# Kernel tuning notes

Hardware: AMD Instinct MI355X
Metric: run time of the kernel (lower is better)

Reference implementation:

```python
import jax, jax.numpy as jnp
import numpy as np

DIM = 768
HEADS = 12
DIM_HEAD = 64
INNER = HEADS * DIM_HEAD  # 768
SCALE = DIM_HEAD ** -0.5


def setup_inputs() -> dict:
    key = jax.random.key(0)
    k1, k2, k3, k4 = jax.random.split(key, 4)
    b, n = 8, 1024
    x = jax.random.normal(k1, (b, n, DIM), dtype=jnp.float32)
    # fused QKV projection, no bias: y = x @ w_qkv  -> [b, n, 3*inner]
    w_qkv = jax.random.normal(k2, (DIM, 3 * INNER), dtype=jnp.float32) * (DIM ** -0.5)
    # output projection with bias
    w_out = jax.random.normal(k3, (INNER, DIM), dtype=jnp.float32) * (INNER ** -0.5)
    b_out = jax.random.normal(k4, (DIM,), dtype=jnp.float32) * 0.02
    return {"x": x, "w_qkv": w_qkv, "w_out": w_out, "b_out": b_out}


def reference(x, w_qkv, w_out, b_out):
    b, n, _ = x.shape
    qkv = jnp.einsum('bnd,de->bne', x, w_qkv)  # [b, n, 3*inner]
    q, k, v = jnp.split(qkv, 3, axis=-1)
    # 'b n (h d) -> b h n d'
    def split_heads(t):
        return t.reshape(b, n, HEADS, DIM_HEAD).transpose(0, 2, 1, 3)
    q, k, v = split_heads(q), split_heads(k), split_heads(v)
    dots = jnp.einsum('bhid,bhjd->bhij', q, k) * SCALE  # [b, h, n, n]
    attn = jax.nn.softmax(dots, axis=-1)
    out = jnp.einsum('bhij,bhjd->bhid', attn, v)  # [b, h, n, d]
    out = out.transpose(0, 2, 1, 3).reshape(b, n, INNER)  # 'b h n d -> b n (h d)'
    return jnp.einsum('bne,ed->bnd', out, w_out) + b_out
```

## Files before the change

### kernel.cpp

```cpp
#include <hip/hip_runtime.h>

typedef unsigned short u16;
typedef __bf16 bf16x8 __attribute__((ext_vector_type(8)));
typedef float f32x4 __attribute__((ext_vector_type(4)));

__device__ inline u16 f2bf(float f) {
    union { float f; unsigned int u; } a; a.f = f;
    unsigned int u = a.u + 0x7fffu + ((a.u >> 16) & 1u);
    return (u16)(u >> 16);
}
__device__ __forceinline__ float truncbf(float f, u16& h) {
    union { float f; unsigned int u; } a; a.f = f;
    a.u &= 0xffff0000u;
    h = (u16)(a.u >> 16);
    return a.f;
}

__device__ __forceinline__ void cp16(const void* g, void* l) {
    __builtin_amdgcn_global_load_lds(
        (const __attribute__((address_space(1))) unsigned int*)g,
        (__attribute__((address_space(3))) unsigned int*)l, 16, 0, 0);
}

__global__ __launch_bounds__(256) void prep(
    const float* __restrict__ x, const float* __restrict__ wq,
    const float* __restrict__ wo, u16* __restrict__ xbf,
    u16* __restrict__ wtq, u16* __restrict__ wto)
{
    int bid = blockIdx.x;
    if (bid < 3072) {
        size_t base = ((size_t)bid * 256 + threadIdx.x) * 8;
        float4 f0 = *(const float4*)&x[base];
        float4 f1 = *(const float4*)&x[base + 4];
        union { u16 s[8]; uint4 v; } t;
        t.s[0]=f2bf(f0.x); t.s[1]=f2bf(f0.y); t.s[2]=f2bf(f0.z); t.s[3]=f2bf(f0.w);
        t.s[4]=f2bf(f1.x); t.s[5]=f2bf(f1.y); t.s[6]=f2bf(f1.z); t.s[7]=f2bf(f1.w);
        *(uint4*)&xbf[base] = t.v;
        return;
    }
    __shared__ u16 tile[32][33];
    const float* in; u16* outp; int N, bx, by;
    if (bid < 3072 + 1728) { int t = bid - 3072; in = wq; outp = wtq; N = 2304; bx = t % 72; by = t / 72; }
    else                   { int t = bid - 4800; in = wo; outp = wto; N = 768;  bx = t % 24; by = t / 24; }
    int n0 = bx * 32, k0 = by * 32;
    int tx = threadIdx.x & 31, ty = threadIdx.x >> 5;
    #pragma unroll
    for (int r = ty; r < 32; r += 8)
        tile[r][tx] = f2bf(in[(size_t)(k0 + r) * N + n0 + tx]);
    __syncthreads();
    #pragma unroll
    for (int r = ty; r < 32; r += 8)
        outp[(size_t)(n0 + r) * 768 + k0 + tx] = tile[tx][r];
}

__global__ __launch_bounds__(256) void gemm_qkv(
    const u16* __restrict__ A, const u16* __restrict__ Bt,
    u16* __restrict__ q_out, u16* __restrict__ k_out, u16* __restrict__ v_out)
{
    const int K = 768;
    __shared__ __align__(16) u16 As[2][128 * 64];
    __shared__ __align__(16) u16 Bs[2][128 * 64];

    int tid = threadIdx.x;
    int lane = tid & 63, wave = tid >> 6;
    int quad = lane >> 4, l16 = lane & 15;
    int wm = wave >> 1, wn = wave & 1;
    int id = blockIdx.x;
    int xcd = id & 7, j = id >> 3;
    int m0 = (((j & 7) << 3) + xcd) * 128;
    int n0 = (j >> 3) * 128;

    f32x4 acc[4][4];
    #pragma unroll
    for (int i = 0; i < 4; i++)
        #pragma unroll
        for (int jj = 0; jj < 4; jj++) acc[i][jj] = (f32x4){0.f, 0.f, 0.f, 0.f};

    int r0 = tid >> 3, cg = tid & 7;
    int g = cg ^ (r0 & 7);
    const u16* GA[4]; const u16* GB[4];
    #pragma unroll
    for (int it = 0; it < 4; it++) {
        GA[it] = A  + (size_t)(m0 + it * 32 + r0) * K + g * 8;
        GB[it] = Bt + (size_t)(n0 + it * 32 + r0) * K + g * 8;
    }

    #define STAGE_QKV(kt, b)                                          \
        _Pragma("unroll")                                             \
        for (int it = 0; it < 4; it++) {                              \
            cp16(GA[it] + (kt), &As[b][(it * 256 + tid) * 8]);        \
            cp16(GB[it] + (kt), &Bs[b][(it * 256 + tid) * 8]);        \
        }

    STAGE_QKV(0, 0)
    for (int i = 0; i < 12; i++) {
        int b = i & 1;
        if (i + 1 < 12) {
            STAGE_QKV((i + 1) * 64, b ^ 1)
            asm volatile("s_waitcnt vmcnt(8)" ::: "memory");
        } else {
            asm volatile("s_waitcnt vmcnt(0)" ::: "memory");
        }
        __builtin_amdgcn_s_barrier();
        bf16x8 af[2][4], bfr[2][4];
        #pragma unroll
        for (int ko = 0; ko < 2; ko++)
            #pragma unroll
            for (int x = 0; x < 4; x++) {
                int Ra = wm * 64 + x * 16 + l16;
                af[ko][x]  = *(const bf16x8*)&As[b][Ra * 64 + (((ko * 4 + quad) ^ (Ra & 7)) * 8)];
                int Rb = wn * 64 + x * 16 + l16;
                bfr[ko][x] = *(const bf16x8*)&Bs[b][Rb * 64 + (((ko * 4 + quad) ^ (Rb & 7)) * 8)];
            }
        #pragma unroll
        for (int ko = 0; ko < 2; ko++)
            #pragma unroll
            for (int x = 0; x < 4; x++)
                #pragma unroll
                for (int y = 0; y < 4; y++)
                    acc[x][y] = __builtin_amdgcn_mfma_f32_16x16x32_bf16(af[ko][x], bfr[ko][y], acc[x][y], 0, 0, 0);
        __builtin_amdgcn_s_barrier();
    }
    #undef STAGE_QKV

    int M0 = m0 + wm * 64, N0 = n0 + wn * 64;
    int part = N0 >= 1536 ? 2 : (N0 >= 768 ? 1 : 0);
    int h = (N0 - part * 768) >> 6;
    int b2 = M0 >> 10, npos0 = M0 & 1023;
    u16* ep = (wave < 2 ? As[0] : Bs[0]) + (wave & 1) * 4096;

    if (part != 2) {
        float scale = (part == 0) ? 0.18033688011112042f : 1.0f;
        u16* gbase = (part == 0 ? q_out : k_out) + (((size_t)(b2 * 12 + h) * 1024 + npos0) << 6);
        #pragma unroll
        for (int i = 0; i < 4; i++)
            #pragma unroll
            for (int jj = 0; jj < 4; jj++) {
                int dd = jj * 16 + l16;
                #pragma unroll
                for (int r = 0; r < 4; r++) {
                    int np = i * 16 + quad * 4 + r;
                    ep[np * 64 + (((dd >> 3) ^ (np & 7)) * 8) + (dd & 7)] =
                        f2bf(acc[i][jj][r] * scale);
                }
            }
        #pragma unroll
        for (int t = 0; t < 8; t++) {
            int idx = t * 512 + lane * 8;
            int np = idx >> 6;
            int slot = ((lane & 7) ^ (np & 7));
            uint4 v = *(const uint4*)&ep[np * 64 + slot * 8];
            *(uint4*)&gbase[idx] = v;
        }
    } else {
        #pragma unroll
        for (int i = 0; i < 4; i++)
            #pragma unroll
            for (int jj = 0; jj < 4; jj++) {
                int dd = jj * 16 + l16;
                int npg = i * 2 + (quad >> 1);
                int sub = (quad & 1) * 4;
                union { u16 s[4]; uint2 v; } pk;
                #pragma unroll
                for (int r = 0; r < 4; r++) pk.s[r] = f2bf(acc[i][jj][r]);
                *(uint2*)&ep[dd * 64 + ((npg ^ (dd & 7)) * 8) + sub] = pk.v;
            }
        #pragma unroll
        for (int t = 0; t < 8; t++) {
            int dd = t * 8 + (lane >> 3);
            int npg = lane & 7;
            uint4 v = *(const uint4*)&ep[dd * 64 + ((npg ^ (dd & 7)) * 8)];
            *(uint4*)&v_out[((size_t)((b2 * 12 + h) * 64 + dd)) * 1024 + npos0 + npg * 8] = v;
        }
    }
}

__global__ __launch_bounds__(256) void attn128(
    u16* __restrict__ QO, const u16* __restrict__ Kg, const u16* __restrict__ Vtg)
{
    __shared__ __align__(16) u16 Ks[2][64 * 64];
    __shared__ __align__(16) u16 Vs[2][64 * 64];

    int tid = threadIdx.x;
    int lane = tid & 63, wave = tid >> 6;
    int quad = lane >> 4, l16 = lane & 15;
    int id = blockIdx.x;
    int xcd = id & 7, j = id >> 3;
    int bh = xcd * 12 + (j >> 3);
    int q0 = (j & 7) * 128;
    const size_t head_base = (size_t)bh * 65536;

    size_t qoff[2];
    bf16x8 qf[2][2];
    #pragma unroll
    for (int qs = 0; qs < 2; qs++) {
        qoff[qs] = head_base + (size_t)(q0 + wave * 32 + qs * 16 + l16) * 64;
        qf[qs][0] = *(const bf16x8*)&QO[qoff[qs] + quad * 8];
        qf[qs][1] = *(const bf16x8*)&QO[qoff[qs] + 32 + quad * 8];
    }

    f32x4 Oacc[4][2];
    #pragma unroll
    for (int dt = 0; dt < 4; dt++)
        #pragma unroll
        for (int qs = 0; qs < 2; qs++) Oacc[dt][qs] = (f32x4){0.f, 0.f, 0.f, 0.f};
    float l_part[2] = {0.f, 0.f};

    int srow = tid >> 3, sg = tid & 7;
    int gs = sg ^ (srow & 7);
    const u16* GK[2]; const u16* GV[2];
    #pragma unroll
    for (int it = 0; it < 2; it++) {
        GK[it] = Kg  + head_base + (size_t)(it * 32 + srow) * 64 + gs * 8;
        GV[it] = Vtg + head_base + (size_t)(it * 32 + srow) * 1024 + gs * 8;
    }

    #define STAGE_ATT(j0, b)                                          \
        _Pragma("unroll")                                             \
        for (int it = 0; it < 2; it++) {                              \
            cp16(GK[it] + (size_t)(j0) * 64, &Ks[b][(it * 256 + tid) * 8]); \
            cp16(GV[it] + (j0),             &Vs[b][(it * 256 + tid) * 8]); \
        }

    STAGE_ATT(0, 0)
    for (int i = 0; i < 16; i++) {
        int b = i & 1;
        if (i + 1 < 16) {
            STAGE_ATT((i + 1) * 64, b ^ 1)
            asm volatile("s_waitcnt vmcnt(4)" ::: "memory");
        } else {
            asm volatile("s_waitcnt vmcnt(0)" ::: "memory");
        }
        __builtin_amdgcn_s_barrier();
        bf16x8 kf[4][2];
        #pragma unroll
        for (int nt = 0; nt < 4; nt++) {
            int R = nt * 16 + l16;
            kf[nt][0] = *(const bf16x8*)&Ks[b][R * 64 + ((quad       ^ (R & 7)) * 8)];
            kf[nt][1] = *(const bf16x8*)&Ks[b][R * 64 + (((quad + 4) ^ (R & 7)) * 8)];
        }

        f32x4 s4[4][2];
        #pragma unroll
        for (int nt = 0; nt < 4; nt++)
            #pragma unroll
            for (int qs = 0; qs < 2; qs++) {
                f32x4 s = (f32x4){0.f, 0.f, 0.f, 0.f};
                s = __builtin_amdgcn_mfma_f32_16x16x32_bf16(kf[nt][0], qf[qs][0], s, 0, 0, 0);
                s = __builtin_amdgcn_mfma_f32_16x16x32_bf16(kf[nt][1], qf[qs][1], s, 0, 0, 0);
                s4[nt][qs] = s;
            }

        u16 ph[4][2][4];
        #pragma unroll
        for (int nt = 0; nt < 4; nt++)
            #pragma unroll
            for (int qs = 0; qs < 2; qs++)
                #pragma unroll
                for (int r = 0; r < 4; r++) {
                    float p = __builtin_amdgcn_exp2f(s4[nt][qs][r]);
                    l_part[qs] += truncbf(p, ph[nt][qs][r]);
                }

        #pragma unroll
        for (int h = 0; h < 2; h++) {
            union { u16 s[8]; bf16x8 v; } pk[2];
            #pragma unroll
            for (int qs = 0; qs < 2; qs++)
                #pragma unroll
                for (int r = 0; r < 4; r++) {
                    pk[qs].s[r]     = ph[2 * h][qs][r];
                    pk[qs].s[4 + r] = ph[2 * h + 1][qs][r];
                }
            int lg0 = 4 * h + (quad >> 1), lg1 = lg0 + 2;
            int off = (quad & 1) * 4;
            #pragma unroll
            for (int dt = 0; dt < 4; dt++) {
                int drow = dt * 16 + l16;
                union { u16 s[8]; bf16x8 v; } vk;
                *(uint2*)&vk.s[0] = *(const uint2*)&Vs[b][drow * 64 + (lg0 ^ (drow & 7)) * 8 + off];
                *(uint2*)&vk.s[4] = *(const uint2*)&Vs[b][drow * 64 + (lg1 ^ (drow & 7)) * 8 + off];
                #pragma unroll
                for (int qs = 0; qs < 2; qs++)
                    Oacc[dt][qs] = __builtin_amdgcn_mfma_f32_16x16x32_bf16(vk.v, pk[qs].v, Oacc[dt][qs], 0, 0, 0);
            }
        }
        __builtin_amdgcn_s_barrier();
    }
    #undef STAGE_ATT

    #pragma unroll
    for (int qs = 0; qs < 2; qs++) {
        float l = l_part[qs];
        l += __shfl_xor(l, 16);
        l += __shfl_xor(l, 32);
        float rl = __builtin_amdgcn_rcpf(l);
        #pragma unroll
        for (int dt = 0; dt < 4; dt++) {
            union { u16 s[4]; uint2 v; } ok;
            #pragma unroll
            for (int r = 0; r < 4; r++) ok.s[r] = f2bf(Oacc[dt][qs][r] * rl);
            *(uint2*)&QO[qoff[qs] + dt * 16 + quad * 4] = ok.v;
        }
    }
}

__global__ __launch_bounds__(256) void gemm_out(
    const u16* __restrict__ Qg, const u16* __restrict__ Bt,
    const float* __restrict__ bias, float* __restrict__ out)
{
    const int K = 768;
    __shared__ __align__(16) u16 As[2][128 * 64];
    __shared__ __align__(16) u16 Bs[2][128 * 64];

    int tid = threadIdx.x;
    int lane = tid & 63, wave = tid >> 6;
    int quad = lane >> 4, l16 = lane & 15;
    int wm = wave >> 1, wn = wave & 1;
    int id = blockIdx.x;
    int xcd = id & 7, j = id >> 3;
    int m0 = (((j & 7) << 3) + xcd) * 128;
    int n0 = (j >> 3) * 128;

    f32x4 acc[4][4];
    #pragma unroll
    for (int i = 0; i < 4; i++)
        #pragma unroll
        for (int jj = 0; jj < 4; jj++) acc[i][jj] = (f32x4){0.f, 0.f, 0.f, 0.f};

    int r0 = tid >> 3, cg = tid & 7;
    int g = cg ^ (r0 & 7);
    const u16* GA[4]; const u16* GB[4];
    #pragma unroll
    for (int it = 0; it < 4; it++) {
        int m = m0 + it * 32 + r0, b = m >> 10, npos = m & 1023;
        GA[it] = Qg + (((size_t)(b * 12) * 1024 + npos) << 6) + g * 8;
        GB[it] = Bt + (size_t)(n0 + it * 32 + r0) * K + g * 8;
    }

    #define STAGE_OUT(i2, b)                                              \
        _Pragma("unroll")                                                 \
        for (int it = 0; it < 4; it++) {                                  \
            cp16(GA[it] + (size_t)(i2) * 65536, &As[b][(it * 256 + tid) * 8]); \
            cp16(GB[it] + (i2) * 64,            &Bs[b][(it * 256 + tid) * 8]); \
        }

    STAGE_OUT(0, 0)
    for (int i = 0; i < 12; i++) {
        int b = i & 1;
        if (i + 1 < 12) {
            STAGE_OUT(i + 1, b ^ 1)
            asm volatile("s_waitcnt vmcnt(8)" ::: "memory");
        } else {
            asm volatile("s_waitcnt vmcnt(0)" ::: "memory");
        }
        __builtin_amdgcn_s_barrier();
        bf16x8 af[2][4], bfr[2][4];
        #pragma unroll
        for (int ko = 0; ko < 2; ko++)
            #pragma unroll
            for (int x = 0; x < 4; x++) {
                int Ra = wm * 64 + x * 16 + l16;
                af[ko][x]  = *(const bf16x8*)&As[b][Ra * 64 + (((ko * 4 + quad) ^ (Ra & 7)) * 8)];
                int Rb = wn * 64 + x * 16 + l16;
                bfr[ko][x] = *(const bf16x8*)&Bs[b][Rb * 64 + (((ko * 4 + quad) ^ (Rb & 7)) * 8)];
            }
        #pragma unroll
        for (int ko = 0; ko < 2; ko++)
            #pragma unroll
            for (int x = 0; x < 4; x++)
                #pragma unroll
                for (int y = 0; y < 4; y++)
                    acc[x][y] = __builtin_amdgcn_mfma_f32_16x16x32_bf16(af[ko][x], bfr[ko][y], acc[x][y], 0, 0, 0);
        __builtin_amdgcn_s_barrier();
    }
    #undef STAGE_OUT

    #pragma unroll
    for (int i = 0; i < 4; i++) {
        int mbase = m0 + wm * 64 + i * 16 + quad * 4;
        #pragma unroll
        for (int jj = 0; jj < 4; jj++) {
            int n = n0 + wn * 64 + jj * 16 + l16;
            float bv = bias[n];
            #pragma unroll
            for (int r = 0; r < 4; r++)
                out[(size_t)(mbase + r) * 768 + n] = acc[i][jj][r] + bv;
        }
    }
}

extern "C" void kernel_launch(void* const* d_in, const int* in_sizes, int n_in,
                              void* d_out, int out_size, void* d_ws, size_t ws_size,
                              hipStream_t stream) {
    const float* x     = (const float*)d_in[0];
    const float* w_qkv = (const float*)d_in[1];
    const float* w_out = (const float*)d_in[2];
    const float* b_out = (const float*)d_in[3];
    float* out = (float*)d_out;

    char* ws = (char*)d_ws;
    u16* wtq  = (u16*)(ws);
    u16* wto  = (u16*)(ws + 3538944);
    u16* Qbuf = (u16*)(ws + 4718592);
    u16* xbf  = (u16*)(ws + 17301504);
    u16* Kbuf = (u16*)d_out;
    u16* Vbuf = (u16*)d_out + 6291456;

    prep<<<dim3(5376), 256, 0, stream>>>(x, w_qkv, w_out, xbf, wtq, wto);
    gemm_qkv<<<dim3(1152), 256, 0, stream>>>(xbf, wtq, Qbuf, Kbuf, Vbuf);
    attn128<<<dim3(768), 256, 0, stream>>>(Qbuf, Kbuf, Vbuf);
    gemm_out<<<dim3(384), 256, 0, stream>>>(Qbuf, wto, b_out, out);
}
```

Measured before the change: 182.8 us.

## Register-stage V tiles with 4-word swizzle, compute row sums via MFMA

V tiles are now loaded into registers and written to LDS with a finer 16-way XOR swizzle after the exp step, instead of using direct global-to-LDS copies. This removes bank conflicts in the PV operand reads and overlaps the LDS writes with compute. Softmax row sums are now accumulated with an extra MFMA against a ones vector, replacing scalar adds and the final shuffles. Probabilities are packed with v_cvt_pk_bf16_f32, which rounds rather than truncates, and s_setprio is raised around the PV MFMAs. In exchange the kernel uses more registers and adds MFMA work plus extra waitcnt points.

Measured after the change: 192.4 us. 1.05x slower.

```diff
diff --git a/kernel.cpp b/kernel.cpp
--- a/kernel.cpp
+++ b/kernel.cpp
@@ -8,12 +8,6 @@
     union { float f; unsigned int u; } a; a.f = f;
     unsigned int u = a.u + 0x7fffu + ((a.u >> 16) & 1u);
     return (u16)(u >> 16);
-}
-__device__ __forceinline__ float truncbf(float f, u16& h) {
-    union { float f; unsigned int u; } a; a.f = f;
-    a.u &= 0xffff0000u;
-    h = (u16)(a.u >> 16);
-    return a.f;
 }
 
 __device__ __forceinline__ void cp16(const void* g, void* l) {
@@ -204,34 +198,54 @@
     for (int dt = 0; dt < 4; dt++)
         #pragma unroll
         for (int qs = 0; qs < 2; qs++) Oacc[dt][qs] = (f32x4){0.f, 0.f, 0.f, 0.f};
-    float l_part[2] = {0.f, 0.f};
+    f32x4 lacc[2];
+    lacc[0] = (f32x4){0.f, 0.f, 0.f, 0.f};
+    lacc[1] = (f32x4){0.f, 0.f, 0.f, 0.f};
+
+    union { unsigned int w[4]; bf16x8 v; } ones;
+    ones.w[0] = ones.w[1] = ones.w[2] = ones.w[3] = 0x3f803f80u;
 
     int srow = tid >> 3, sg = tid & 7;
-    int gs = sg ^ (srow & 7);
-    const u16* GK[2]; const u16* GV[2];
+    int gsK = sg ^ (srow & 7);
+    const u16* GK[2];
+    GK[0] = Kg + head_base + (size_t)(srow) * 64 + gsK * 8;
+    GK[1] = Kg + head_base + (size_t)(32 + srow) * 64 + gsK * 8;
+    const u16* GV[2];
+    GV[0] = Vtg + head_base + (size_t)(srow) * 1024 + sg * 8;
+    GV[1] = Vtg + head_base + (size_t)(32 + srow) * 1024 + sg * 8;
+    int vwA[2], vwB[2];
     #pragma unroll
     for (int it = 0; it < 2; it++) {
-        GK[it] = Kg  + head_base + (size_t)(it * 32 + srow) * 64 + gs * 8;
-        GV[it] = Vtg + head_base + (size_t)(it * 32 + srow) * 1024 + gs * 8;
-    }
-
-    #define STAGE_ATT(j0, b)                                          \
-        _Pragma("unroll")                                             \
-        for (int it = 0; it < 2; it++) {                              \
-            cp16(GK[it] + (size_t)(j0) * 64, &Ks[b][(it * 256 + tid) * 8]); \
-            cp16(GV[it] + (j0),             &Vs[b][(it * 256 + tid) * 8]); \
-        }
-
-    STAGE_ATT(0, 0)
+        int r = it * 32 + srow;
+        vwA[it] = r * 64 + (((2 * sg)     ^ (r & 15)) * 4);
+        vwB[it] = r * 64 + (((2 * sg + 1) ^ (r & 15)) * 4);
+    }
+
+    uint4 v0a = *(const uint4*)GV[0];
+    uint4 v0b = *(const uint4*)GV[1];
+    cp16(GK[0], &Ks[0][(0 * 256 + tid) * 8]);
+    cp16(GK[1], &Ks[0][(1 * 256 + tid) * 8]);
+    { uint2 t;
+      t.x = v0a.x; t.y = v0a.y; *(uint2*)&Vs[0][vwA[0]] = t;
+      t.x = v0a.z; t.y = v0a.w; *(uint2*)&Vs[0][vwB[0]] = t;
+      t.x = v0b.x; t.y = v0b.y; *(uint2*)&Vs[0][vwA[1]] = t;
+      t.x = v0b.z; t.y = v0b.w; *(uint2*)&Vs[0][vwB[1]] = t; }
+    asm volatile("s_waitcnt lgkmcnt(0)" ::: "memory");
+
     for (int i = 0; i < 16; i++) {
         int b = i & 1;
+        uint4 vna, vnb;
         if (i + 1 < 16) {
-            STAGE_ATT((i + 1) * 64, b ^ 1)
+            vna = *(const uint4*)(GV[0] + (i + 1) * 64);
+            vnb = *(const uint4*)(GV[1] + (i + 1) * 64);
+            cp16(GK[0] + (size_t)(i + 1) * 4096, &Ks[b ^ 1][(0 * 256 + tid) * 8]);
+            cp16(GK[1] + (size_t)(i + 1) * 4096, &Ks[b ^ 1][(1 * 256 + tid) * 8]);
             asm volatile("s_waitcnt vmcnt(4)" ::: "memory");
         } else {
             asm volatile("s_waitcnt vmcnt(0)" ::: "memory");
         }
         __builtin_amdgcn_s_barrier();
+
         bf16x8 kf[4][2];
         #pragma unroll
         for (int nt = 0; nt < 4; nt++) {
@@ -239,7 +253,6 @@
             kf[nt][0] = *(const bf16x8*)&Ks[b][R * 64 + ((quad       ^ (R & 7)) * 8)];
             kf[nt][1] = *(const bf16x8*)&Ks[b][R * 64 + (((quad + 4) ^ (R & 7)) * 8)];
         }
-
         f32x4 s4[4][2];
         #pragma unroll
         for (int nt = 0; nt < 4; nt++)
@@ -251,50 +264,57 @@
                 s4[nt][qs] = s;
             }
 
-        u16 ph[4][2][4];
+        float p[4][2][4];
         #pragma unroll
         for (int nt = 0; nt < 4; nt++)
             #pragma unroll
             for (int qs = 0; qs < 2; qs++)
                 #pragma unroll
-                for (int r = 0; r < 4; r++) {
-                    float p = __builtin_amdgcn_exp2f(s4[nt][qs][r]);
-                    l_part[qs] += truncbf(p, ph[nt][qs][r]);
-                }
-
+                for (int r = 0; r < 4; r++)
+                    p[nt][qs][r] = __builtin_amdgcn_exp2f(s4[nt][qs][r]);
+
+        if (i + 1 < 16) {
+            asm volatile("s_waitcnt vmcnt(2)" ::: "memory");
+            uint2 t;
+            t.x = vna.x; t.y = vna.y; *(uint2*)&Vs[b ^ 1][vwA[0]] = t;
+            t.x = vna.z; t.y = vna.w; *(uint2*)&Vs[b ^ 1][vwB[0]] = t;
+            t.x = vnb.x; t.y = vnb.y; *(uint2*)&Vs[b ^ 1][vwA[1]] = t;
+            t.x = vnb.z; t.y = vnb.w; *(uint2*)&Vs[b ^ 1][vwB[1]] = t;
+        }
+
+        __builtin_amdgcn_s_setprio(1);
         #pragma unroll
         for (int h = 0; h < 2; h++) {
-            union { u16 s[8]; bf16x8 v; } pk[2];
-            #pragma unroll
-            for (int qs = 0; qs < 2; qs++)
-                #pragma unroll
-                for (int r = 0; r < 4; r++) {
-                    pk[qs].s[r]     = ph[2 * h][qs][r];
-                    pk[qs].s[4 + r] = ph[2 * h + 1][qs][r];
-                }
-            int lg0 = 4 * h + (quad >> 1), lg1 = lg0 + 2;
-            int off = (quad & 1) * 4;
+            union { unsigned int w[4]; bf16x8 v; } pk[2];
+            #pragma unroll
+            for (int qs = 0; qs < 2; qs++) {
+                asm("v_cvt_pk_bf16_f32 %0, %1, %2" : "=v"(pk[qs].w[0]) : "v"(p[2*h][qs][0]),     "v"(p[2*h][qs][1]));
+                asm("v_cvt_pk_bf16_f32 %0, %1, %2" : "=v"(pk[qs].w[1]) : "v"(p[2*h][qs][2]),     "v"(p[2*h][qs][3]));
+                asm("v_cvt_pk_bf16_f32 %0, %1, %2" : "=v"(pk[qs].w[2]) : "v"(p[2*h+1][qs][0]),   "v"(p[2*h+1][qs][1]));
+                asm("v_cvt_pk_bf16_f32 %0, %1, %2" : "=v"(pk[qs].w[3]) : "v"(p[2*h+1][qs][2]),   "v"(p[2*h+1][qs][3]));
+                lacc[qs] = __builtin_amdgcn_mfma_f32_16x16x32_bf16(ones.v, pk[qs].v, lacc[qs], 0, 0, 0);
+            }
+            int pbase = ((8 * h + quad) ^ l16) * 4;
             #pragma unroll
             for (int dt = 0; dt < 4; dt++) {
                 int drow = dt * 16 + l16;
                 union { u16 s[8]; bf16x8 v; } vk;
-                *(uint2*)&vk.s[0] = *(const uint2*)&Vs[b][drow * 64 + (lg0 ^ (drow & 7)) * 8 + off];
-                *(uint2*)&vk.s[4] = *(const uint2*)&Vs[b][drow * 64 + (lg1 ^ (drow & 7)) * 8 + off];
+                *(uint2*)&vk.s[0] = *(const uint2*)&Vs[b][drow * 64 + pbase];
+                *(uint2*)&vk.s[4] = *(const uint2*)&Vs[b][drow * 64 + (pbase ^ 16)];
                 #pragma unroll
                 for (int qs = 0; qs < 2; qs++)
                     Oacc[dt][qs] = __builtin_amdgcn_mfma_f32_16x16x32_bf16(vk.v, pk[qs].v, Oacc[dt][qs], 0, 0, 0);
             }
         }
-        __builtin_amdgcn_s_barrier();
-    }
-    #undef STAGE_ATT
+        __builtin_amdgcn_s_setprio(0);
+
+        asm volatile("s_waitcnt lgkmcnt(0)" ::: "memory");
+        __builtin_amdgcn_s_barrier();
+    }
 
     #pragma unroll
     for (int qs = 0; qs < 2; qs++) {
-        float l = l_part[qs];
-        l += __shfl_xor(l, 16);
-        l += __shfl_xor(l, 32);
-        float rl = __builtin_amdgcn_rcpf(l);
+        float rl = __builtin_amdgcn_rcpf(lacc[qs][0]);
         #pragma unroll
         for (int dt = 0; dt < 4; dt++) {
             union { u16 s[4]; uint2 v; } ok;
```
